# Optimization experiments

Measured on AMD Instinct MI355X. Metric: run time of the kernel, lower is better.

The kernel has to match this reference:

```python
import jax, jax.numpy as jnp
import numpy as np

B, N, D, K = 1024, 36, 256, 8  # batch, num_features(fixed 36 by docstring), embed_size, text_K


def setup_inputs() -> dict:
    key = jax.random.key(0)
    ks = jax.random.split(key, 5)
    texts = jax.random.normal(ks[0], (B, N, D), dtype=jnp.float32)
    # Xavier-uniform-style init matching module.init_weights()
    r_k = np.sqrt(6.0) / np.sqrt(D + D)
    r_v = np.sqrt(6.0) / np.sqrt(D + K)
    r_u = np.sqrt(6.0) / np.sqrt(K + 1)
    W = jax.random.uniform(ks[1], (K, D, D), minval=-r_k, maxval=r_k, dtype=jnp.float32)
    Wb = jnp.zeros((K, D), dtype=jnp.float32)
    V1w = jax.random.uniform(ks[2], (K, D), minval=-r_v, maxval=r_v, dtype=jnp.float32)
    V1b = jnp.zeros((K,), dtype=jnp.float32)
    V2w = jax.random.uniform(ks[3], (K, D), minval=-r_v, maxval=r_v, dtype=jnp.float32)
    V2b = jnp.zeros((K,), dtype=jnp.float32)
    Uw = jax.random.uniform(ks[4], (K,), minval=-r_u, maxval=r_u, dtype=jnp.float32)
    Ub = jnp.zeros((), dtype=jnp.float32)
    return {"texts": texts, "W": W, "Wb": Wb, "V1w": V1w, "V1b": V1b,
            "V2w": V2w, "V2b": V2b, "Uw": Uw, "Ub": Ub}


def reference(texts, W, Wb, V1w, V1b, V2w, V2b, Uw, Ub):
    # bilinear term: (W_k x_n + b_k) . x_m  -> [B,K,N,N]
    Wx = jnp.einsum('kcd,bnd->bknc', W, texts) + Wb[None, :, None, :]
    first = jnp.einsum('bknc,bmc->bknm', Wx, texts)
    # outer-sum term: V1.x_n + V2.x_m (per k)
    v1 = jnp.einsum('kd,bnd->bkn', V1w, texts) + V1b[None, :, None]  # [B,K,N]
    v2 = jnp.einsum('kd,bmd->bkm', V2w, texts) + V2b[None, :, None]  # [B,K,N]
    T = jnp.tanh(first + v1[..., None] + v2[:, :, None, :])  # [B,K,N,N]
    # faithful to torch: flatten [K,N,N] contiguously then view as (N*N, K)
    flat = T.reshape(T.shape[0], N * N, K)
    logits = (flat @ Uw + Ub).reshape(T.shape[0], N, N)
    return jax.nn.softmax(logits, axis=-1)
```

## Files before the change

kernel.cpp:

```cpp
#include <hip/hip_runtime.h>
#include <math.h>

#define NB 1024
#define NF 36
#define ED 256
#define NK 8
#define NN2 1296

typedef _Float16 f16;
typedef f16 f16x4 __attribute__((ext_vector_type(4)));
typedef f16 f16x8 __attribute__((ext_vector_type(8)));
typedef float f32x4 __attribute__((ext_vector_type(4)));

#define WXSTR 136
#define NFRAG 1536

#define XC2_OFF 16384
#define ZB_OFF  18432
#define WX0_OFF 18448
#define WX1_OFF (WX0_OFF + 9792)
#define V_OFF   (WX1_OFF + 9792)
#define SMEM_MAIN (V_OFF + (72 + 72 + 9 + 324) * 4)

#define PVH_OFF 0
#define PVL_OFF 8192
#define PP_OFF  16384
#define SMEM_PREP 28672

#define TWO_LOG2E 2.8853900817779268f
#define C1F (0.0625f * TWO_LOG2E)

__device__ __forceinline__ f32x4 mfma16(f16x8 a, f16x8 b, f32x4 c) {
    return __builtin_amdgcn_mfma_f32_16x16x32_f16(a, b, c, 0, 0, 0);
}

__device__ __forceinline__ const f16x8* xfragp(const char* smem, int f, int lane) {
    const int l15 = lane & 15, q = (lane >> 4) & 3;
    int off;
    if (f < 16) off = (f * 64 + lane) * 16;
    else        off = (l15 < 4) ? (XC2_OFF + (((f - 16) * 16) + q * 4 + l15) * 16)
                                : ZB_OFF;
    return (const f16x8*)(smem + off);
}

__global__ __launch_bounds__(256, 4) void prep_all(
    const float* __restrict__ W, f16x8* __restrict__ WfH,
    const float* __restrict__ texts, f16x8* __restrict__ XfH,
    const float* __restrict__ V1w, const float* __restrict__ V1b,
    const float* __restrict__ V2w, const float* __restrict__ V2b,
    const float* __restrict__ Wb, float* __restrict__ v12)
{
    extern __shared__ char psmem[];
    const int blk = blockIdx.x;
    const int t = threadIdx.x;
    const int wave = t >> 6, lane = t & 63;

    if (blk < 128) {
        const int k = blk >> 4, ct = blk & 15;
        f16* Wl = (f16*)psmem;
        {
            const int r = t >> 4, seg = t & 15;
            const float* src = W + ((size_t)(k * 256 + ct * 16 + r)) * 256 + seg * 16;
            f16* d = Wl + r * 264 + seg * 16;
            #pragma unroll
            for (int j4 = 0; j4 < 4; ++j4) {
                float4 a = ((const float4*)src)[j4];
                d[j4 * 4 + 0] = (f16)(a.x * 16.0f);
                d[j4 * 4 + 1] = (f16)(a.y * 16.0f);
                d[j4 * 4 + 2] = (f16)(a.z * 16.0f);
                d[j4 * 4 + 3] = (f16)(a.w * 16.0f);
            }
        }
        __syncthreads();
        f16x8* dst = WfH + (size_t)(k * 16 + ct) * 8 * 64;
        #pragma unroll
        for (int e0 = 0; e0 < 2; ++e0) {
            const int e = t + e0 * 256;
            const int kc = e >> 6, el = e & 63, qd = el >> 4, l15 = el & 15;
            dst[e] = *(const f16x8*)(Wl + l15 * 264 + (kc * 4 + qd) * 8);
        }
        return;
    }

    f16x8* VfH = (f16x8*)(psmem + PVH_OFF);
    f16x8* VfL = (f16x8*)(psmem + PVL_OFF);
    f32x4* Pp  = (f32x4*)(psmem + PP_OFF);

    const int b = blk - 128;
    const float* xb = texts + (size_t)b * NF * ED;

    #pragma unroll
    for (int i0 = 0; i0 < 2; ++i0) {
        int i = t + i0 * 256;
        int kc = (i >> 6) & 7, ln = i & 63;
        int q = ln >> 4, col = ln & 15;
        int which = col >> 3, kk = col & 7;
        const float* src  = (which ? V2w : V1w) + kk * 256 + kc * 32 + q * 8;
        const float* srcb = Wb + kk * 256 + kc * 32 + q * 8;
        f16x8 hi, lo;
        #pragma unroll
        for (int j = 0; j < 8; ++j) {
            float sv = src[j] + (which ? srcb[j] : 0.f);
            sv *= 16.0f;
            f16 h = (f16)sv;
            hi[j] = h;
            lo[j] = (f16)(sv - (float)h);
        }
        VfH[i] = hi;
        VfL[i] = lo;
    }

    f16x8 FH[6], FL[6];
    #pragma unroll
    for (int i0 = 0; i0 < 6; ++i0) {
        int i = t + i0 * 256;
        int rt = i >> 9, kc = (i >> 6) & 7;
        int q = lane >> 4, l15 = lane & 15;
        int row = rt * 16 + l15;
        f16x8 hi, lo;
        if (row < NF) {
            const float* s = xb + row * ED + kc * 32 + q * 8;
            float4 a = *(const float4*)s;
            float4 c = *(const float4*)(s + 4);
            float v[8] = {a.x, a.y, a.z, a.w, c.x, c.y, c.z, c.w};
            #pragma unroll
            for (int j = 0; j < 8; ++j) {
                f16 h = (f16)v[j];
                hi[j] = h;
                lo[j] = (f16)(v[j] - (float)h);
            }
        } else {
            #pragma unroll
            for (int j = 0; j < 8; ++j) { hi[j] = (f16)0.f; lo[j] = (f16)0.f; }
        }
        FH[i0] = hi;
        FL[i0] = lo;
        XfH[(size_t)b * NFRAG + i] = hi;
    }
    __syncthreads();

    f32x4 pacc[3];
    #pragma unroll
    for (int rt = 0; rt < 3; ++rt) pacc[rt] = (f32x4){0.f, 0.f, 0.f, 0.f};
    #pragma unroll
    for (int rt = 0; rt < 3; ++rt) {
        #pragma unroll
        for (int s = 0; s < 2; ++s) {
            const int i0 = rt * 2 + s;
            const int kc = wave + 4 * s;
            f16x8 bh = VfH[kc * 64 + lane];
            f16x8 bl = VfL[kc * 64 + lane];
            pacc[rt] = mfma16(FH[i0], bh, pacc[rt]);
            pacc[rt] = mfma16(FH[i0], bl, pacc[rt]);
            pacc[rt] = mfma16(FL[i0], bh, pacc[rt]);
        }
    }
    #pragma unroll
    for (int rt = 0; rt < 3; ++rt)
        Pp[(wave * 3 + rt) * 64 + lane] = pacc[rt];
    __syncthreads();

    if (wave < 3) {
        f32x4 acc = Pp[(0 * 3 + wave) * 64 + lane];
        #pragma unroll
        for (int w = 1; w < 4; ++w) acc += Pp[(w * 3 + wave) * 64 + lane];
        const int q = lane >> 4, l15 = lane & 15;
        const int which = l15 >> 3, kk = l15 & 7;
        const float bias = which ? V2b[kk] : V1b[kk];
        #pragma unroll
        for (int r = 0; r < 4; ++r) {
            const int n = wave * 16 + q * 4 + r;
            if (n < NF)
                v12[((size_t)b * 16 + l15) * NF + n] = acc[r] * 0.0625f + bias;
        }
    }
}

#define P1S(ACC, H, KC) do {                                                  \
    f16x8 w00_ = Wk0[((((H) * 8 + wave) * 8) + (KC)) * 64 + lane];            \
    f16x8 w01_ = Wk0[((((H) * 8 + wave + 4) * 8) + (KC)) * 64 + lane];        \
    f16x8 w10_ = Wk1[((((H) * 8 + wave) * 8) + (KC)) * 64 + lane];            \
    f16x8 w11_ = Wk1[((((H) * 8 + wave + 4) * 8) + (KC)) * 64 + lane];        \
    _Pragma("unroll")                                                         \
    for (int rt_ = 0; rt_ < 3; ++rt_) {                                       \
        f16x8 ah_ = *xfragp(smem, rt_ * 8 + (KC), lane);                      \
        ACC[rt_][0][0] = mfma16(w00_, ah_, ACC[rt_][0][0]);                   \
        ACC[rt_][1][0] = mfma16(w01_, ah_, ACC[rt_][1][0]);                   \
        ACC[rt_][0][1] = mfma16(w10_, ah_, ACC[rt_][0][1]);                   \
        ACC[rt_][1][1] = mfma16(w11_, ah_, ACC[rt_][1][1]);                   \
    }                                                                         \
} while (0)

#define P2_TILE2(IT, H) do {                                                  \
    const int p_ = wave + (IT) * 4;                                           \
    if (p_ < 9) {                                                             \
        const int nt_ = p_ / 3, mt_ = p_ % 3;                                 \
        const int row_ = nt_ * 16 + l15;                                      \
        const int cr_ = row_ > 35 ? 35 : row_;    \
        const f16* w0p_ = Wxh0 + cr_ * WXSTR + quad * 8;                      \
        const f16* w1p_ = Wxh1 + cr_ * WXSTR + quad * 8;                      \
        _Pragma("unroll")                                                     \
        for (int kc2_ = 0; kc2_ < 4; ++kc2_) {                                \
            f16x8 xb_ = *xfragp(smem, mt_ * 8 + (H) * 4 + kc2_, lane);        \
            f16x8 a0_ = *(const f16x8*)(w0p_ + kc2_ * 32);                    \
            f16x8 a1_ = *(const f16x8*)(w1p_ + kc2_ * 32);                    \
            sacc[0][IT] = mfma16(a0_, xb_, sacc[0][IT]);                      \
            sacc[1][IT] = mfma16(a1_, xb_, sacc[1][IT]);                      \
        }                                                                     \
    }                                                                         \
} while (0)

#define ZERO_ACC(ACC) do {                                                    \
    _Pragma("unroll")                                                         \
    for (int i_ = 0; i_ < 3; ++i_)                                            \
        _Pragma("unroll")                                                     \
        for (int j_ = 0; j_ < 2; ++j_) {                                      \
            ACC[i_][j_][0] = (f32x4){0.f, 0.f, 0.f, 0.f};                     \
            ACC[i_][j_][1] = (f32x4){0.f, 0.f, 0.f, 0.f};                     \
        }                                                                     \
} while (0)

#define STORE_WX2(ACC) do {                                                   \
    _Pragma("unroll")                                                         \
    for (int rt_ = 0; rt_ < 3; ++rt_) {                                       \
        const int n_ = rt_ * 16 + l15;                                        \
        if (rt_ < 2 || l15 < 4) {                                             \
            _Pragma("unroll")                                                 \
            for (int j2_ = 0; j2_ < 2; ++j2_) {                               \
                const int cb_ = (j2_ ? (wave + 4) : wave) * 16 + quad * 4;    \
                f16x4 h0_, h1_;                                               \
                _Pragma("unroll")                                             \
                for (int r_ = 0; r_ < 4; ++r_) {                              \
                    h0_[r_] = (f16)(ACC[rt_][j2_][0][r_]);                    \
                    h1_[r_] = (f16)(ACC[rt_][j2_][1][r_]);                    \
                }                                                             \
                *(f16x4*)(Wxh0 + n_ * WXSTR + cb_) = h0_;                     \
                *(f16x4*)(Wxh1 + n_ * WXSTR + cb_) = h1_;                     \
            }                                                                 \
        }                                                                     \
    }                                                                         \
} while (0)

__global__ __launch_bounds__(256, 4) void ntn_main(
    const f16x8* __restrict__ XfHG,
    const f16x8* __restrict__ WfH,
    const float* __restrict__ v12,
    const float* __restrict__ Uw, const float* __restrict__ Ubp,
    float* __restrict__ out)
{
    extern __shared__ char smem[];
    f16*   Wxh0 = (f16*)(smem + WX0_OFF);
    f16*   Wxh1 = (f16*)(smem + WX1_OFF);
    float* v1s2 = (float*)(smem + V_OFF);
    float* v2s2 = v1s2 + 72;
    float* Uws  = v1s2 + 144;
    float* Ls   = v1s2 + 153;

    const int id  = blockIdx.x;
    const int xcd = id & 7;
    const int rem = id >> 3;
    const int kp  = rem & 3;
    const int b   = ((rem >> 2) << 3) | xcd;
    const int k0  = kp * 2;

    const int t    = threadIdx.x;
    const int wave = t >> 6;
    const int lane = t & 63;
    const int quad = lane >> 4;
    const int l15  = lane & 15;

    {
        const f16x8* gh = XfHG + (size_t)b * NFRAG;
        #pragma unroll
        for (int i0 = 0; i0 < 4; ++i0)
            *(f16x8*)(smem + (size_t)(t + i0 * 256) * 16) = gh[t + i0 * 256];
        #pragma unroll
        for (int i0 = 4; i0 < 6; ++i0) {
            const int e = t + i0 * 256;
            f16x8 v = gh[e];
            const int kc = (e >> 6) - 16;
            if (l15 < 4)
                *(f16x8*)(smem + XC2_OFF + (size_t)(kc * 16 + quad * 4 + l15) * 16) = v;
        }
        if (t == 0) {
            f16x8 z;
            #pragma unroll
            for (int j = 0; j < 8; ++j) z[j] = (f16)0.f;
            *(f16x8*)(smem + ZB_OFF) = z;
        }
    }
    if (t < 144) {
        const int r = t / 36, n = t - r * 36;
        const int which = r & 1, kq = r >> 1;
        float v = v12[((size_t)b * 16 + which * 8 + (k0 + kq)) * NF + n] * TWO_LOG2E;
        (which ? v2s2 : v1s2)[kq * 36 + n] = v;
    }
    if (t < 8) Uws[t] = Uw[t];
    if (t == 8) Uws[8] = Ubp[0];
    __syncthreads();

    const f16x8* Wk0 = WfH + (size_t)k0 * 8192;
    const f16x8* Wk1 = Wk0 + 8192;

    f32x4 sacc[2][3];
    #pragma unroll
    for (int kk = 0; kk < 2; ++kk)
        #pragma unroll
        for (int it = 0; it < 3; ++it) sacc[kk][it] = (f32x4){0.f, 0.f, 0.f, 0.f};

    f32x4 acc[3][2][2];

    ZERO_ACC(acc);
    #pragma unroll
    for (int kc = 0; kc < 8; ++kc) P1S(acc, 0, kc);
    STORE_WX2(acc);
    __syncthreads();

    ZERO_ACC(acc);
    #pragma unroll
    for (int kc = 0; kc < 8; ++kc) {
        P1S(acc, 1, kc);
        if (kc == 1) P2_TILE2(0, 0);
        if (kc == 3) P2_TILE2(1, 0);
        if (kc == 5) P2_TILE2(2, 0);
    }
    __syncthreads();
    STORE_WX2(acc);
    __syncthreads();

    P2_TILE2(0, 1);
    P2_TILE2(1, 1);
    P2_TILE2(2, 1);

    __syncthreads();
    float* Ts = (float*)Wxh0;
    #pragma unroll
    for (int kk = 0; kk < 2; ++kk)
        #pragma unroll
        for (int it = 0; it < 3; ++it) {
            const int p = wave + it * 4;
            if (p < 9) {
                const int nt = p / 3, mt = p % 3;
                const int m = mt * 16 + l15;
                if (m < NF) {
                    #pragma unroll
                    for (int r = 0; r < 4; ++r) {
                        const int n = nt * 16 + quad * 4 + r;
                        if (n < NF) {
                            float x = sacc[kk][it][r] * C1F
                                      + v1s2[kk * 36 + n] + v2s2[kk * 36 + m];
                            float e = exp2f(x);
                            const int idx = kk * NN2 + n * NF + m;
                            Ts[idx + (idx >> 3)] = 1.f - 2.f / (e + 1.f);
                        }
                    }
                }
            }
        }
    __syncthreads();
    #pragma unroll
    for (int u0 = 0; u0 < 2; ++u0) {
        const int u = t + u0 * 256;
        if (u < 324) {
            const float* tp = Ts + u * 9;
            float lg = Uws[8];
            #pragma unroll
            for (int j = 0; j < 8; ++j) lg += Uws[j] * tp[j];
            Ls[u] = lg;
        }
    }
    __syncthreads();
    #pragma unroll
    for (int rr0 = 0; rr0 < 3; ++rr0) {
        const int rr = wave + rr0 * 4;
        if (rr < 9) {
            float v = (lane < NF) ? Ls[rr * 36 + lane] : -INFINITY;
            float mx = v;
            #pragma unroll
            for (int off = 32; off > 0; off >>= 1) mx = fmaxf(mx, __shfl_xor(mx, off));
            float e = (lane < NF) ? __expf(v - mx) : 0.f;
            float sm = e;
            #pragma unroll
            for (int off = 32; off > 0; off >>= 1) sm += __shfl_xor(sm, off);
            if (lane < NF)
                out[(size_t)b * NN2 + kp * 324 + rr * 36 + lane] = e / sm;
        }
    }
}

extern "C" void kernel_launch(void* const* d_in, const int* in_sizes, int n_in,
                              void* d_out, int out_size, void* d_ws, size_t ws_size,
                              hipStream_t stream) {
    const float* texts = (const float*)d_in[0];
    const float* W     = (const float*)d_in[1];
    const float* Wb    = (const float*)d_in[2];
    const float* V1w   = (const float*)d_in[3];
    const float* V1b   = (const float*)d_in[4];
    const float* V2w   = (const float*)d_in[5];
    const float* V2b   = (const float*)d_in[6];
    const float* Uw    = (const float*)d_in[7];
    const float* Ub    = (const float*)d_in[8];

    char* ws = (char*)d_ws;
    f16x8* WfH = (f16x8*)ws;
    f16x8* XfH = (f16x8*)(ws + (1 << 20));
    float* v12 = (float*)(ws + (1 << 20) + (size_t)NB * NFRAG * 16);
    float* outp = (float*)d_out;

    hipFuncSetAttribute((const void*)prep_all,
                        hipFuncAttributeMaxDynamicSharedMemorySize, SMEM_PREP);
    hipFuncSetAttribute((const void*)ntn_main,
                        hipFuncAttributeMaxDynamicSharedMemorySize, SMEM_MAIN);

    prep_all<<<128 + NB, 256, SMEM_PREP, stream>>>(W, WfH, texts, XfH,
                                                   V1w, V1b, V2w, V2b, Wb, v12);
    ntn_main<<<NB * NK / 2, 256, SMEM_MAIN, stream>>>(XfH, WfH, v12, Uw, Ub, outp);
}
```

Measured before the change: 190.5 us.

## Restructure bilinear stage to process one k per phase with full-width Wx buffer

```diff
diff --git a/kernel.cpp b/kernel.cpp
--- a/kernel.cpp
+++ b/kernel.cpp
@@ -12,14 +12,13 @@
 typedef f16 f16x8 __attribute__((ext_vector_type(8)));
 typedef float f32x4 __attribute__((ext_vector_type(4)));
 
-#define WXSTR 136
+#define WXSTR 264
 #define NFRAG 1536
 
 #define XC2_OFF 16384
 #define ZB_OFF  18432
-#define WX0_OFF 18448
-#define WX1_OFF (WX0_OFF + 9792)
-#define V_OFF   (WX1_OFF + 9792)
+#define WX_OFF  18448
+#define V_OFF   (WX_OFF + 19008)
 #define SMEM_MAIN (V_OFF + (72 + 72 + 9 + 324) * 4)
 
 #define PVH_OFF 0
@@ -176,66 +175,57 @@
     }
 }
 
-#define P1S(ACC, H, KC) do {                                                  \
-    f16x8 w00_ = Wk0[((((H) * 8 + wave) * 8) + (KC)) * 64 + lane];            \
-    f16x8 w01_ = Wk0[((((H) * 8 + wave + 4) * 8) + (KC)) * 64 + lane];        \
-    f16x8 w10_ = Wk1[((((H) * 8 + wave) * 8) + (KC)) * 64 + lane];            \
-    f16x8 w11_ = Wk1[((((H) * 8 + wave + 4) * 8) + (KC)) * 64 + lane];        \
+#define P1F(WKP, KC) do {                                                     \
+    f16x8 w0_ = (WKP)[(((0 * 4 + wave) * 8) + (KC)) * 64 + lane];             \
+    f16x8 w1_ = (WKP)[(((1 * 4 + wave) * 8) + (KC)) * 64 + lane];             \
+    f16x8 w2_ = (WKP)[(((2 * 4 + wave) * 8) + (KC)) * 64 + lane];             \
+    f16x8 w3_ = (WKP)[(((3 * 4 + wave) * 8) + (KC)) * 64 + lane];             \
     _Pragma("unroll")                                                         \
     for (int rt_ = 0; rt_ < 3; ++rt_) {                                       \
         f16x8 ah_ = *xfragp(smem, rt_ * 8 + (KC), lane);                      \
-        ACC[rt_][0][0] = mfma16(w00_, ah_, ACC[rt_][0][0]);                   \
-        ACC[rt_][1][0] = mfma16(w01_, ah_, ACC[rt_][1][0]);                   \
-        ACC[rt_][0][1] = mfma16(w10_, ah_, ACC[rt_][0][1]);                   \
-        ACC[rt_][1][1] = mfma16(w11_, ah_, ACC[rt_][1][1]);                   \
+        acc[rt_][0] = mfma16(w0_, ah_, acc[rt_][0]);                          \
+        acc[rt_][1] = mfma16(w1_, ah_, acc[rt_][1]);                          \
+        acc[rt_][2] = mfma16(w2_, ah_, acc[rt_][2]);                          \
+        acc[rt_][3] = mfma16(w3_, ah_, acc[rt_][3]);                          \
     }                                                                         \
 } while (0)
 
-#define P2_TILE2(IT, H) do {                                                  \
+#define P2T(IT, KK) do {                                                      \
     const int p_ = wave + (IT) * 4;                                           \
     if (p_ < 9) {                                                             \
         const int nt_ = p_ / 3, mt_ = p_ % 3;                                 \
         const int row_ = nt_ * 16 + l15;                                      \
-        const int cr_ = row_ > 35 ? 35 : row_;    \
-        const f16* w0p_ = Wxh0 + cr_ * WXSTR + quad * 8;                      \
-        const f16* w1p_ = Wxh1 + cr_ * WXSTR + quad * 8;                      \
+        const int cr_ = row_ > 35 ? 35 : row_;           \
+        const f16* wp_ = Wxh + cr_ * WXSTR + quad * 8;                        \
         _Pragma("unroll")                                                     \
-        for (int kc2_ = 0; kc2_ < 4; ++kc2_) {                                \
-            f16x8 xb_ = *xfragp(smem, mt_ * 8 + (H) * 4 + kc2_, lane);        \
-            f16x8 a0_ = *(const f16x8*)(w0p_ + kc2_ * 32);                    \
-            f16x8 a1_ = *(const f16x8*)(w1p_ + kc2_ * 32);                    \
-            sacc[0][IT] = mfma16(a0_, xb_, sacc[0][IT]);                      \
-            sacc[1][IT] = mfma16(a1_, xb_, sacc[1][IT]);                      \
+        for (int kc2_ = 0; kc2_ < 8; ++kc2_) {                                \
+            f16x8 pah_ = *(const f16x8*)(wp_ + kc2_ * 32);                    \
+            f16x8 pbh_ = *xfragp(smem, mt_ * 8 + kc2_, lane);                 \
+            sacc[KK][IT] = mfma16(pah_, pbh_, sacc[KK][IT]);                  \
         }                                                                     \
     }                                                                         \
 } while (0)
 
-#define ZERO_ACC(ACC) do {                                                    \
+#define ZERO_ACC() do {                                                       \
     _Pragma("unroll")                                                         \
     for (int i_ = 0; i_ < 3; ++i_)                                            \
         _Pragma("unroll")                                                     \
-        for (int j_ = 0; j_ < 2; ++j_) {                                      \
-            ACC[i_][j_][0] = (f32x4){0.f, 0.f, 0.f, 0.f};                     \
-            ACC[i_][j_][1] = (f32x4){0.f, 0.f, 0.f, 0.f};                     \
-        }                                                                     \
+        for (int j_ = 0; j_ < 4; ++j_)                                        \
+            acc[i_][j_] = (f32x4){0.f, 0.f, 0.f, 0.f};                        \
 } while (0)
 
-#define STORE_WX2(ACC) do {                                                   \
+#define STORE_WXF() do {                                                      \
     _Pragma("unroll")                                                         \
     for (int rt_ = 0; rt_ < 3; ++rt_) {                                       \
         const int n_ = rt_ * 16 + l15;                                        \
         if (rt_ < 2 || l15 < 4) {                                             \
             _Pragma("unroll")                                                 \
-            for (int j2_ = 0; j2_ < 2; ++j2_) {                               \
-                const int cb_ = (j2_ ? (wave + 4) : wave) * 16 + quad * 4;    \
-                f16x4 h0_, h1_;                                               \
+            for (int j_ = 0; j_ < 4; ++j_) {                                  \
+                const int cb_ = (j_ * 4 + wave) * 16 + quad * 4;              \
+                f16x4 h4_;                                                    \
                 _Pragma("unroll")                                             \
-                for (int r_ = 0; r_ < 4; ++r_) {                              \
-                    h0_[r_] = (f16)(ACC[rt_][j2_][0][r_]);                    \
-                    h1_[r_] = (f16)(ACC[rt_][j2_][1][r_]);                    \
-                }                                                             \
-                *(f16x4*)(Wxh0 + n_ * WXSTR + cb_) = h0_;                     \
-                *(f16x4*)(Wxh1 + n_ * WXSTR + cb_) = h1_;                     \
+                for (int r_ = 0; r_ < 4; ++r_) h4_[r_] = (f16)(acc[rt_][j_][r_]); \
+                *(f16x4*)(Wxh + n_ * WXSTR + cb_) = h4_;                      \
             }                                                                 \
         }                                                                     \
     }                                                                         \
@@ -249,8 +239,7 @@
     float* __restrict__ out)
 {
     extern __shared__ char smem[];
-    f16*   Wxh0 = (f16*)(smem + WX0_OFF);
-    f16*   Wxh1 = (f16*)(smem + WX1_OFF);
+    f16*   Wxh  = (f16*)(smem + WX_OFF);
     float* v1s2 = (float*)(smem + V_OFF);
     float* v2s2 = v1s2 + 72;
     float* Uws  = v1s2 + 144;
@@ -308,32 +297,30 @@
         #pragma unroll
         for (int it = 0; it < 3; ++it) sacc[kk][it] = (f32x4){0.f, 0.f, 0.f, 0.f};
 
-    f32x4 acc[3][2][2];
-
-    ZERO_ACC(acc);
-    #pragma unroll
-    for (int kc = 0; kc < 8; ++kc) P1S(acc, 0, kc);
-    STORE_WX2(acc);
-    __syncthreads();
-
-    ZERO_ACC(acc);
-    #pragma unroll
-    for (int kc = 0; kc < 8; ++kc) {
-        P1S(acc, 1, kc);
-        if (kc == 1) P2_TILE2(0, 0);
-        if (kc == 3) P2_TILE2(1, 0);
-        if (kc == 5) P2_TILE2(2, 0);
-    }
-    __syncthreads();
-    STORE_WX2(acc);
-    __syncthreads();
-
-    P2_TILE2(0, 1);
-    P2_TILE2(1, 1);
-    P2_TILE2(2, 1);
-
-    __syncthreads();
-    float* Ts = (float*)Wxh0;
+    f32x4 acc[3][4];
+
+    ZERO_ACC();
+    #pragma unroll
+    for (int kc = 0; kc < 8; ++kc) P1F(Wk0, kc);
+    STORE_WXF();
+    __syncthreads();
+
+    P2T(0, 0);
+    P2T(1, 0);
+    P2T(2, 0);
+    ZERO_ACC();
+    #pragma unroll
+    for (int kc = 0; kc < 8; ++kc) P1F(Wk1, kc);
+    __syncthreads();
+    STORE_WXF();
+    __syncthreads();
+
+    P2T(0, 1);
+    P2T(1, 1);
+    P2T(2, 1);
+
+    __syncthreads();
+    float* Ts = (float*)Wxh;
     #pragma unroll
     for (int kk = 0; kk < 2; ++kk)
         #pragma unroll
```

Result: slower. 196.0 us (+2.9%).
